# Optimization experiments

Measured on AMD Instinct MI355X. Metric: run time of the kernel, lower is better.

Reference implementation:

```python
import jax, jax.numpy as jnp
import numpy as np

C = 256

def setup_inputs() -> dict:
    key = jax.random.key(0)
    ks = jax.random.split(key, 7)
    s = 1.0 / np.sqrt(C)
    x = jax.random.normal(ks[0], (4, C, 64, 64), dtype=jnp.float32)
    Wq = jax.random.uniform(ks[1], (C, C), jnp.float32, -s, s)
    bq = jax.random.uniform(ks[2], (C,), jnp.float32, -s, s)
    Wk = jax.random.uniform(ks[3], (C, C), jnp.float32, -s, s)
    bk = jax.random.uniform(ks[4], (C,), jnp.float32, -s, s)
    Wv = jax.random.uniform(ks[5], (C, C), jnp.float32, -s, s)
    bv = jax.random.uniform(ks[6], (C,), jnp.float32, -s, s)
    return {"x": x, "Wq": Wq, "bq": bq, "Wk": Wk, "bk": bk, "Wv": Wv, "bv": bv}

def reference(x, Wq, bq, Wk, bk, Wv, bv):
    B, Cc, H, W = x.shape
    N = H * W
    xf = x.reshape(B, Cc, N)                      # (B, C, N)
    # 1x1 conv == channel linear: out[b,o,n] = sum_c W[o,c] x[b,c,n] + b[o]
    q = jnp.einsum('oc,bcn->bno', Wq, xf) + bq    # (B, N, C)  proj_query^T
    k = jnp.einsum('oc,bcn->bon', Wk, xf) + bk[None, :, None]  # (B, C, N)
    v = jnp.einsum('oc,bcn->bon', Wv, xf) + bv[None, :, None]  # (B, C, N)
    energy = jnp.einsum('bnc,bcm->bnm', q, k)     # (B, N, N)
    attention = jax.nn.softmax(energy, axis=-1)
    # out = V @ attention^T : out[b,c,n] = sum_m v[b,c,m] * attention[b,n,m]
    out = jnp.einsum('bcm,bnm->bcn', v, attention)
    return out.reshape(B, Cc, H, W)
```

## Files before the change

kernel.cpp:

```cpp
#include <hip/hip_runtime.h>
#include <math.h>

#define BB 4
#define CC 256
#define NN 4096
#define KV 64

using half8 = __attribute__((ext_vector_type(8))) _Float16;
using f32x4 = __attribute__((ext_vector_type(4))) float;
using f32x16 = __attribute__((ext_vector_type(16))) float;

__device__ __forceinline__ unsigned short f2h(float f) {
  _Float16 h = (_Float16)f;
  return __builtin_bit_cast(unsigned short, h);
}
__device__ __forceinline__ float h2f(unsigned short u) {
  return (float)__builtin_bit_cast(_Float16, u);
}

#define ASYNC16(g, l)                                                        \
  __builtin_amdgcn_global_load_lds(                                          \
      (const __attribute__((address_space(1))) unsigned int*)(g),            \
      (__attribute__((address_space(3))) unsigned int*)(l), 16, 0, 0)

__device__ __forceinline__ int vt_off(int r, int chunk) {
  return r * 64 + (((chunk ^ r) & 7) << 3);
}

__global__ __launch_bounds__(256) void k_wcast(const float* __restrict__ Wq,
    const float* __restrict__ Wk, const float* __restrict__ Wv,
    unsigned short* __restrict__ Wt) {
  int id = blockIdx.x * 256 + threadIdx.x;
  int pos8 = id & 7, o = (id >> 3) & 255, ks = (id >> 11) & 3, p3 = id >> 13;
  const float* W = p3 == 0 ? Wq : (p3 == 1 ? Wk : Wv);
  int c = ks * 64 + ((pos8 ^ o) & 7) * 8;
  const float* src = W + (size_t)o * CC + c;
  float4 a = *(const float4*)(src);
  float4 b4 = *(const float4*)(src + 4);
  union { unsigned short u[8]; uint4 v4; } pk;
  pk.u[0] = f2h(a.x);  pk.u[1] = f2h(a.y);  pk.u[2] = f2h(a.z);  pk.u[3] = f2h(a.w);
  pk.u[4] = f2h(b4.x); pk.u[5] = f2h(b4.y); pk.u[6] = f2h(b4.z); pk.u[7] = f2h(b4.w);
  *(uint4*)(Wt + (size_t)id * 8) = pk.v4;
}

__global__ __launch_bounds__(512) void k_proj(const float* __restrict__ x,
    const unsigned short* __restrict__ Wt,
    const float* __restrict__ bq, const float* __restrict__ bk,
    const float* __restrict__ bv,
    unsigned short* __restrict__ Q, unsigned short* __restrict__ K,
    unsigned short* __restrict__ V) {
  __shared__ __align__(16) char ps[110848];
  float* xf = (float*)ps;
  unsigned short* xa = (unsigned short*)(ps + 8448);
  unsigned short* wh = (unsigned short*)(ps + 12544);
  int b = blockIdx.y, n0 = blockIdx.x * 32;
  int t = threadIdx.x, w = t >> 6, lane = t & 63, l15 = lane & 15, quad = lane >> 4;

  f32x4 z = {0.f, 0.f, 0.f, 0.f};
  f32x4 acc[3][2][2];
#pragma unroll
  for (int p3 = 0; p3 < 3; ++p3)
#pragma unroll
    for (int ct = 0; ct < 2; ++ct)
#pragma unroll
      for (int mt = 0; mt < 2; ++mt) acc[p3][ct][mt] = z;

  for (int ks = 0; ks < 4; ++ks) {
    if (ks) __syncthreads();
#pragma unroll
    for (int p3 = 0; p3 < 3; ++p3) {
      const char* wb = (const char*)(Wt + (size_t)(p3 * 4 + ks) * 16384);
#pragma unroll
      for (int p = 0; p < 4; ++p) {
        int c = p * 512 + t;
        ASYNC16(wb + c * 16, &wh[p3 * 16384 + (p * 512 + (w << 6)) * 8]);
      }
    }
    {
      int c = t >> 3, nl = (t & 7) * 4;
      float4 v = *(const float4*)(x + ((size_t)b * CC + ks * 64 + c) * NN + n0 + nl);
      float* d = xf + c * 33 + nl;
      d[0] = v.x; d[1] = v.y; d[2] = v.z; d[3] = v.w;
    }
    __syncthreads();
    {
      int n = t >> 4, cb = (t & 15) * 4;
      union { unsigned short u[4]; ushort4 v4; } tmp;
#pragma unroll
      for (int i = 0; i < 4; ++i) tmp.u[i] = f2h(xf[(cb + i) * 33 + n]);
      int ch = cb >> 3;
      *(ushort4*)&xa[n * 64 + (((ch ^ n) & 7) << 3) + (cb & 7)] = tmp.v4;
    }
    __syncthreads();
#pragma unroll
    for (int kc = 0; kc < 2; ++kc) {
      half8 af[2];
#pragma unroll
      for (int mt = 0; mt < 2; ++mt)
        af[mt] = *(const half8*)&xa[vt_off(mt * 16 + l15, kc * 4 + quad)];
#pragma unroll
      for (int p3 = 0; p3 < 3; ++p3)
#pragma unroll
        for (int ct = 0; ct < 2; ++ct) {
          half8 bf = *(const half8*)&wh[p3 * 16384 + vt_off(w * 32 + ct * 16 + l15, kc * 4 + quad)];
#pragma unroll
          for (int mt = 0; mt < 2; ++mt)
            acc[p3][ct][mt] = __builtin_amdgcn_mfma_f32_16x16x32_f16(af[mt], bf, acc[p3][ct][mt], 0, 0, 0);
        }
    }
  }
#pragma unroll
  for (int p3 = 0; p3 < 3; ++p3) {
    const float* bias = p3 == 0 ? bq : (p3 == 1 ? bk : bv);
#pragma unroll
    for (int ct = 0; ct < 2; ++ct) {
      float bv_ = bias[w * 32 + ct * 16 + l15];
#pragma unroll
      for (int mt = 0; mt < 2; ++mt)
#pragma unroll
        for (int r = 0; r < 4; ++r) acc[p3][ct][mt][r] += bv_;
    }
  }
#pragma unroll
  for (int p3 = 0; p3 < 2; ++p3) {
    __syncthreads();
    unsigned short* qo = (unsigned short*)ps;
#pragma unroll
    for (int ct = 0; ct < 2; ++ct)
#pragma unroll
      for (int mt = 0; mt < 2; ++mt)
#pragma unroll
        for (int r = 0; r < 4; ++r)
          qo[(mt * 16 + quad * 4 + r) * 264 + w * 32 + ct * 16 + l15] = f2h(acc[p3][ct][mt][r]);
    __syncthreads();
    unsigned short* outp = (p3 == 0 ? Q : K) + ((size_t)b * NN + n0) * CC;
#pragma unroll
    for (int p = 0; p < 2; ++p) {
      int f = p * 8192 + t * 16;
      int n = f >> 9, off = f & 511;
      *(uint4*)((char*)outp + (size_t)n * 512 + off) =
        *(const uint4*)((const char*)&qo[n * 264] + off);
    }
  }
  {
    __syncthreads();
    unsigned short* vo = (unsigned short*)ps;
#pragma unroll
    for (int ct = 0; ct < 2; ++ct)
#pragma unroll
      for (int mt = 0; mt < 2; ++mt)
#pragma unroll
        for (int r = 0; r < 4; ++r)
          vo[(w * 32 + ct * 16 + l15) * 36 + mt * 16 + quad * 4 + r] = f2h(acc[2][ct][mt][r]);
    __syncthreads();
#pragma unroll
    for (int p = 0; p < 2; ++p) {
      int id = p * 512 + t;
      int o = id >> 2, off = (id & 3) * 16;
      *(uint4*)((char*)(V + ((size_t)b * CC + o) * NN + n0) + off) =
        *(const uint4*)((const char*)&vo[o * 36] + off);
    }
  }
}

__global__ __launch_bounds__(512, 2) void k_flash(const unsigned short* __restrict__ Q,
    const unsigned short* __restrict__ K, const unsigned short* __restrict__ V,
    float* __restrict__ out, unsigned short* __restrict__ opart,
    float* __restrict__ ml, int n_splits) {
  __shared__ __align__(16) char sm[134144];
  unsigned short* kt0 = (unsigned short*)sm;
  unsigned short* kt1 = (unsigned short*)(sm + 32768);
  unsigned short* vt0 = (unsigned short*)(sm + 65536);
  unsigned short* vt1 = (unsigned short*)(sm + 98304);
  float* mx  = (float*)(sm + 131072);
  float* ll_ = (float*)(sm + 133120);

  int b = blockIdx.y, q0 = blockIdx.x * 128, split = blockIdx.z;
  int nt = (NN / KV) / n_splits;
  int t = threadIdx.x, w = t >> 6, lane = t & 63;
  int qn = lane & 31, hi = lane >> 5;
  int qg = w >> 1, kth = w & 1;

  half8 qf[16];
  {
    const unsigned short* qrow = Q + ((size_t)b * NN + q0 + qg * 32 + qn) * CC;
#pragma unroll
    for (int cs = 0; cs < 16; ++cs)
      qf[cs] = *(const half8*)(qrow + cs * 16 + hi * 8);
  }

  f32x16 o_acc[8];
#pragma unroll
  for (int ct = 0; ct < 8; ++ct)
#pragma unroll
    for (int r = 0; r < 16; ++r) o_acc[ct][r] = 0.f;

  f32x16 sa;
  float m_i = -INFINITY, lp = 0.f, pm_carry = -INFINITY;

  int it_beg = split * nt, it_end = it_beg + nt;

  auto dma_k = [&](int it, unsigned short* dst) {
    const char* kb = (const char*)(K + ((size_t)b * NN + it * KV) * CC);
#pragma unroll
    for (int p = 0; p < 4; ++p) {
      int c = p * 512 + t;
      int r = c >> 5, chp = c & 31;
      ASYNC16(kb + r * 512 + ((chp ^ (r & 31)) << 4), &dst[(p * 512 + (w << 6)) * 8]);
    }
  };
  auto dma_v = [&](int it, unsigned short* dst) {
    const char* vb = (const char*)(V + (size_t)b * CC * NN) + it * 128;
#pragma unroll
    for (int p = 0; p < 4; ++p) {
      int c = p * 512 + t;
      int r = c >> 3, chp = c & 7;
      ASYNC16(vb + (size_t)r * 8192 + ((chp ^ (r & 7)) << 4), &dst[(p * 512 + (w << 6)) * 8]);
    }
  };

  auto qkt = [&](const unsigned short* kc) {
#pragma unroll
    for (int r = 0; r < 16; ++r) sa[r] = 0.f;
    __builtin_amdgcn_s_setprio(1);
#pragma unroll
    for (int cs = 0; cs < 16; ++cs) {
      half8 kf = *(const half8*)&kc[(kth * 32 + qn) * 256 + ((((cs * 2 + hi) ^ qn) & 31) << 3)];
      sa = __builtin_amdgcn_mfma_f32_32x32x16_f16(kf, qf[cs], sa, 0, 0, 0);
    }
    __builtin_amdgcn_s_setprio(0);
  };

  auto partial_max = [&](int par) {
    float pm = sa[0];
#pragma unroll
    for (int r = 1; r < 16; ++r) pm = fmaxf(pm, sa[r]);
    pm = fmaxf(pm, __shfl_xor(pm, 32, 64));
    pm_carry = pm;
    if (lane < 32) mx[(par * 2 + kth) * 128 + qg * 32 + lane] = pm;
  };

  unsigned int g0x, g0y, g1x, g1y, g2x, g2y, g3x, g3y;

  auto finish_sm = [&](int prevpar) {
    float prt = mx[(prevpar * 2 + (kth ^ 1)) * 128 + qg * 32 + qn];
    float mtile = fmaxf(pm_carry, prt);
    float mnew = fmaxf(m_i, mtile);
    float alpha = __expf(m_i - mnew);
    m_i = mnew;
    float ls = 0.f;
#pragma unroll
    for (int r = 0; r < 16; ++r) {
      float p = __expf(sa[r] - mnew);
      sa[r] = p;
      ls += p;
    }
    ls += __shfl_xor(ls, 32, 64);
    lp = lp * alpha + ls;
    g0x = (unsigned)f2h(sa[0])  | ((unsigned)f2h(sa[1])  << 16);
    g0y = (unsigned)f2h(sa[2])  | ((unsigned)f2h(sa[3])  << 16);
    g1x = (unsigned)f2h(sa[4])  | ((unsigned)f2h(sa[5])  << 16);
    g1y = (unsigned)f2h(sa[6])  | ((unsigned)f2h(sa[7])  << 16);
    g2x = (unsigned)f2h(sa[8])  | ((unsigned)f2h(sa[9])  << 16);
    g2y = (unsigned)f2h(sa[10]) | ((unsigned)f2h(sa[11]) << 16);
    g3x = (unsigned)f2h(sa[12]) | ((unsigned)f2h(sa[13]) << 16);
    g3y = (unsigned)f2h(sa[14]) | ((unsigned)f2h(sa[15]) << 16);
    if (!__all(alpha == 1.0f)) {
#pragma unroll
      for (int ct = 0; ct < 8; ++ct)
#pragma unroll
        for (int r = 0; r < 16; ++r) o_acc[ct][r] *= alpha;
    }
  };

  auto pv = [&](const unsigned short* vp) {
    __builtin_amdgcn_s_setprio(1);
#pragma unroll
    for (int s = 0; s < 2; ++s) {
      unsigned int ax = s ? g2x : g0x, ay = s ? g2y : g0y;
      unsigned int bx = s ? g3x : g1x, by = s ? g3y : g1y;
      unsigned int vx = hi ? ax : bx, vy = hi ? ay : by;
      unsigned int xx = (unsigned int)__shfl_xor((int)vx, 32, 64);
      unsigned int xy = (unsigned int)__shfl_xor((int)vy, 32, 64);
      union { unsigned int u[4]; half8 h; } bf;
      bf.u[0] = hi ? xx : ax;
      bf.u[1] = hi ? xy : ay;
      bf.u[2] = hi ? bx : xx;
      bf.u[3] = hi ? by : xy;
#pragma unroll
      for (int ct = 0; ct < 8; ++ct) {
        half8 af = *(const half8*)&vp[(ct * 32 + qn) * 64 + ((((kth * 4 + s * 2 + hi) ^ (qn & 7)) & 7) << 3)];
        o_acc[ct] = __builtin_amdgcn_mfma_f32_32x32x16_f16(af, bf.h, o_acc[ct], 0, 0, 0);
      }
    }
    __builtin_amdgcn_s_setprio(0);
  };

  dma_k(it_beg, (it_beg & 1) ? kt1 : kt0);
  dma_v(it_beg, (it_beg & 1) ? vt1 : vt0);
  asm volatile("s_waitcnt vmcnt(4) lgkmcnt(0)" ::: "memory");
  __builtin_amdgcn_s_barrier();
  __builtin_amdgcn_sched_barrier(0);
  {
    int par = it_beg & 1;
    if (it_beg + 1 < it_end) {
      dma_k(it_beg + 1, par ? kt0 : kt1);
      dma_v(it_beg + 1, par ? vt0 : vt1);
    }
    qkt(par ? kt1 : kt0);
    partial_max(par);
  }
  for (int it = it_beg + 1; it < it_end; ++it) {
    int par = it & 1;
    const unsigned short* kcur = par ? kt1 : kt0;
    unsigned short* knxt = par ? kt0 : kt1;
    unsigned short* vprv = par ? vt0 : vt1;
    asm volatile("s_waitcnt vmcnt(4) lgkmcnt(0)" ::: "memory");
    __builtin_amdgcn_s_barrier();
    __builtin_amdgcn_sched_barrier(0);
    if (it + 1 < it_end) dma_k(it + 1, knxt);
    finish_sm(par ^ 1);
    pv(vprv);
    __builtin_amdgcn_sched_barrier(0);
    __builtin_amdgcn_s_barrier();
    __builtin_amdgcn_sched_barrier(0);
    if (it + 1 < it_end) dma_v(it + 1, vprv);
    qkt(kcur);
    partial_max(par);
  }
  __syncthreads();
  {
    int par = (it_end - 1) & 1;
    finish_sm(par);
    pv(par ? vt1 : vt0);
  }

  if (lane < 32) ll_[kth * 128 + qg * 32 + lane] = lp;
  __syncthreads();
  float* od0 = (float*)sm;
  float* od1 = od0 + 32 * 132;
  float* linv = (float*)(sm + 33792);
  if (t < 128) {
    float l = ll_[t] + ll_[128 + t];
    linv[t] = (n_splits == 1) ? 1.0f / l : 1.0f;
  }
  if (n_splits != 1 && kth == 0 && lane < 32) {
    size_t qi = (size_t)q0 + qg * 32 + lane;
    float lt = ll_[qg * 32 + lane] + ll_[128 + qg * 32 + lane];
    ml[((size_t)(split * 2 + 0) * BB + b) * NN + qi] = m_i;
    ml[((size_t)(split * 2 + 1) * BB + b) * NN + qi] = lt;
  }
  __syncthreads();

  float* obf = out + (size_t)b * CC * NN + q0;
  unsigned short* obh = opart + ((size_t)split * BB + b) * CC * NN + q0;
#pragma unroll
  for (int ct = 0; ct < 8; ++ct) {
    float* od = kth ? od1 : od0;
#pragma unroll
    for (int r = 0; r < 16; ++r) {
      int cl = (r & 3) + 8 * (r >> 2) + 4 * hi;
      od[cl * 132 + qg * 32 + qn] = o_acc[ct][r];
    }
    __syncthreads();
    {
      int row = t >> 4, q8 = (t & 15) * 8;
      f32x4 a0 = *(const f32x4*)&od0[row * 132 + q8];
      f32x4 a1 = *(const f32x4*)&od0[row * 132 + q8 + 4];
      f32x4 b0 = *(const f32x4*)&od1[row * 132 + q8];
      f32x4 b1 = *(const f32x4*)&od1[row * 132 + q8 + 4];
      f32x4 l0 = *(const f32x4*)&linv[q8];
      f32x4 l1 = *(const f32x4*)&linv[q8 + 4];
      f32x4 s0, s1;
#pragma unroll
      for (int i = 0; i < 4; ++i) {
        s0[i] = (a0[i] + b0[i]) * l0[i];
        s1[i] = (a1[i] + b1[i]) * l1[i];
      }
      if (n_splits == 1) {
        *(f32x4*)(obf + (size_t)(ct * 32 + row) * NN + q8) = s0;
        *(f32x4*)(obf + (size_t)(ct * 32 + row) * NN + q8 + 4) = s1;
      } else {
        union { unsigned short u[8]; uint4 v4; } tmp;
#pragma unroll
        for (int i = 0; i < 4; ++i) { tmp.u[i] = f2h(s0[i]); tmp.u[4 + i] = f2h(s1[i]); }
        *(uint4*)(obh + (size_t)(ct * 32 + row) * NN + q8) = tmp.v4;
      }
    }
    __syncthreads();
  }
}

__global__ __launch_bounds__(256) void k_merge(const unsigned short* __restrict__ opart,
    const float* __restrict__ ml, float* __restrict__ out) {
  size_t i = ((size_t)blockIdx.x * 256 + threadIdx.x) * 4;
  int n = (int)(i & (NN - 1));
  int b = (int)(i >> 20);
  float4 m1 = *(const float4*)(ml + ((size_t)(0 * BB) + b) * NN + n);
  float4 l1 = *(const float4*)(ml + ((size_t)(1 * BB) + b) * NN + n);
  float4 m2 = *(const float4*)(ml + ((size_t)(2 * BB) + b) * NN + n);
  float4 l2 = *(const float4*)(ml + ((size_t)(3 * BB) + b) * NN + n);
  ushort4 o1 = *(const ushort4*)(opart + i);
  ushort4 o2 = *(const ushort4*)(opart + (size_t)BB * CC * NN + i);
  float4 res;
#define MRG(f, comp) { \
    float M = fmaxf(m1.f, m2.f); \
    float e1 = __expf(m1.f - M), e2 = __expf(m2.f - M); \
    res.f = (e1 * h2f(o1.comp) + e2 * h2f(o2.comp)) / (e1 * l1.f + e2 * l2.f); }
  MRG(x, x) MRG(y, y) MRG(z, z) MRG(w, w)
#undef MRG
  *(float4*)(out + i) = res;
}

extern "C" void kernel_launch(void* const* d_in, const int* in_sizes, int n_in,
                              void* d_out, int out_size, void* d_ws, size_t ws_size,
                              hipStream_t stream) {
  const float* x  = (const float*)d_in[0];
  const float* Wq = (const float*)d_in[1];
  const float* bq = (const float*)d_in[2];
  const float* Wk = (const float*)d_in[3];
  const float* bk = (const float*)d_in[4];
  const float* Wv = (const float*)d_in[5];
  const float* bv = (const float*)d_in[6];
  float* out = (float*)d_out;
  char* ws = (char*)d_ws;
  const size_t MB = 1024 * 1024;
  unsigned short* Qb = (unsigned short*)(ws);
  unsigned short* Kb = (unsigned short*)(ws + 8 * MB);
  unsigned short* Vb = (unsigned short*)(ws + 16 * MB);
  unsigned short* Op = (unsigned short*)(ws + 24 * MB);
  float*          Ml = (float*)(ws + 40 * MB);

  int ns = (ws_size >= 41 * MB) ? 2 : 1;
  unsigned short* Wt = (unsigned short*)(ns == 2 ? ws + 40 * MB + 256 * 1024
                                                 : ws + 24 * MB);

  k_wcast<<<dim3(96), 256, 0, stream>>>(Wq, Wk, Wv, Wt);
  k_proj<<<dim3(128, 4), 512, 0, stream>>>(x, Wt, bq, bk, bv, Qb, Kb, Vb);

  k_flash<<<dim3(32, 4, ns), 512, 0, stream>>>(Qb, Kb, Vb, out, Op, Ml, ns);
  if (ns == 2) k_merge<<<dim3(4096), 256, 0, stream>>>(Op, Ml, out);
}
```

Baseline: 240.4 us.

## Decouple per-wave softmax statistics and adopt lazy rescaling in flash loop

Each of the two key-half waves now keeps its own running max and sum instead of exchanging partial maxima through LDS every tile. The two halves are combined once at the end, and the split-merge kernel is adjusted because partial outputs are now normalized. Rescaling of the accumulator is skipped unless the max grows by more than 8, which trims exp and multiply work. The main loop is rewritten as a simple double-buffered loop with a single barrier per tile. This drops the previous software pipeline that overlapped QK of one tile with softmax and PV of the prior tile, and its fine-grained vmcnt waits, so load latency may be less hidden.

Result: faster. 213.1 us (-11.4%).

```diff
diff --git a/kernel.cpp b/kernel.cpp
--- a/kernel.cpp
+++ b/kernel.cpp
@@ -167,13 +167,13 @@
     const unsigned short* __restrict__ K, const unsigned short* __restrict__ V,
     float* __restrict__ out, unsigned short* __restrict__ opart,
     float* __restrict__ ml, int n_splits) {
-  __shared__ __align__(16) char sm[134144];
+  __shared__ __align__(16) char sm[133120];
   unsigned short* kt0 = (unsigned short*)sm;
   unsigned short* kt1 = (unsigned short*)(sm + 32768);
   unsigned short* vt0 = (unsigned short*)(sm + 65536);
   unsigned short* vt1 = (unsigned short*)(sm + 98304);
-  float* mx  = (float*)(sm + 131072);
-  float* ll_ = (float*)(sm + 133120);
+  float* mm_ = (float*)(sm + 131072);
+  float* ll_ = (float*)(sm + 132096);
 
   int b = blockIdx.y, q0 = blockIdx.x * 128, split = blockIdx.z;
   int nt = (NN / KV) / n_splits;
@@ -195,8 +195,7 @@
 #pragma unroll
     for (int r = 0; r < 16; ++r) o_acc[ct][r] = 0.f;
 
-  f32x16 sa;
-  float m_i = -INFINITY, lp = 0.f, pm_carry = -INFINITY;
+  float m_i = -INFINITY, lp = 0.f;
 
   int it_beg = split * nt, it_end = it_beg + nt;
 
@@ -219,61 +218,64 @@
     }
   };
 
-  auto qkt = [&](const unsigned short* kc) {
+  dma_k(it_beg, (it_beg & 1) ? kt1 : kt0);
+  dma_v(it_beg, (it_beg & 1) ? vt1 : vt0);
+
+  for (int it = it_beg; it < it_end; ++it) {
+    int par = it & 1;
+    const unsigned short* kcur = par ? kt1 : kt0;
+    const unsigned short* vcur = par ? vt1 : vt0;
+
+    __syncthreads();
+
+    if (it + 1 < it_end) {
+      dma_k(it + 1, par ? kt0 : kt1);
+      dma_v(it + 1, par ? vt0 : vt1);
+    }
+
+    f32x16 sa;
 #pragma unroll
     for (int r = 0; r < 16; ++r) sa[r] = 0.f;
     __builtin_amdgcn_s_setprio(1);
 #pragma unroll
     for (int cs = 0; cs < 16; ++cs) {
-      half8 kf = *(const half8*)&kc[(kth * 32 + qn) * 256 + ((((cs * 2 + hi) ^ qn) & 31) << 3)];
+      half8 kf = *(const half8*)&kcur[(kth * 32 + qn) * 256 + ((((cs * 2 + hi) ^ qn) & 31) << 3)];
       sa = __builtin_amdgcn_mfma_f32_32x32x16_f16(kf, qf[cs], sa, 0, 0, 0);
     }
     __builtin_amdgcn_s_setprio(0);
-  };
-
-  auto partial_max = [&](int par) {
+
     float pm = sa[0];
 #pragma unroll
     for (int r = 1; r < 16; ++r) pm = fmaxf(pm, sa[r]);
     pm = fmaxf(pm, __shfl_xor(pm, 32, 64));
-    pm_carry = pm;
-    if (lane < 32) mx[(par * 2 + kth) * 128 + qg * 32 + lane] = pm;
-  };
-
-  unsigned int g0x, g0y, g1x, g1y, g2x, g2y, g3x, g3y;
-
-  auto finish_sm = [&](int prevpar) {
-    float prt = mx[(prevpar * 2 + (kth ^ 1)) * 128 + qg * 32 + qn];
-    float mtile = fmaxf(pm_carry, prt);
-    float mnew = fmaxf(m_i, mtile);
-    float alpha = __expf(m_i - mnew);
-    m_i = mnew;
+    if (!__all(pm <= m_i + 8.0f)) {
+      float mnew = fmaxf(m_i, pm);
+      float alpha = __expf(m_i - mnew);
+      m_i = mnew;
+      lp *= alpha;
+#pragma unroll
+      for (int ct = 0; ct < 8; ++ct)
+#pragma unroll
+        for (int r = 0; r < 16; ++r) o_acc[ct][r] *= alpha;
+    }
     float ls = 0.f;
 #pragma unroll
     for (int r = 0; r < 16; ++r) {
-      float p = __expf(sa[r] - mnew);
+      float p = __expf(sa[r] - m_i);
       sa[r] = p;
       ls += p;
     }
-    ls += __shfl_xor(ls, 32, 64);
-    lp = lp * alpha + ls;
-    g0x = (unsigned)f2h(sa[0])  | ((unsigned)f2h(sa[1])  << 16);
-    g0y = (unsigned)f2h(sa[2])  | ((unsigned)f2h(sa[3])  << 16);
-    g1x = (unsigned)f2h(sa[4])  | ((unsigned)f2h(sa[5])  << 16);
-    g1y = (unsigned)f2h(sa[6])  | ((unsigned)f2h(sa[7])  << 16);
-    g2x = (unsigned)f2h(sa[8])  | ((unsigned)f2h(sa[9])  << 16);
-    g2y = (unsigned)f2h(sa[10]) | ((unsigned)f2h(sa[11]) << 16);
-    g3x = (unsigned)f2h(sa[12]) | ((unsigned)f2h(sa[13]) << 16);
-    g3y = (unsigned)f2h(sa[14]) | ((unsigned)f2h(sa[15]) << 16);
-    if (!__all(alpha == 1.0f)) {
-#pragma unroll
-      for (int ct = 0; ct < 8; ++ct)
-#pragma unroll
-        for (int r = 0; r < 16; ++r) o_acc[ct][r] *= alpha;
-    }
-  };
-
-  auto pv = [&](const unsigned short* vp) {
+    lp += ls;
+
+    unsigned int g0x = (unsigned)f2h(sa[0])  | ((unsigned)f2h(sa[1])  << 16);
+    unsigned int g0y = (unsigned)f2h(sa[2])  | ((unsigned)f2h(sa[3])  << 16);
+    unsigned int g1x = (unsigned)f2h(sa[4])  | ((unsigned)f2h(sa[5])  << 16);
+    unsigned int g1y = (unsigned)f2h(sa[6])  | ((unsigned)f2h(sa[7])  << 16);
+    unsigned int g2x = (unsigned)f2h(sa[8])  | ((unsigned)f2h(sa[9])  << 16);
+    unsigned int g2y = (unsigned)f2h(sa[10]) | ((unsigned)f2h(sa[11]) << 16);
+    unsigned int g3x = (unsigned)f2h(sa[12]) | ((unsigned)f2h(sa[13]) << 16);
+    unsigned int g3y = (unsigned)f2h(sa[14]) | ((unsigned)f2h(sa[15]) << 16);
+
     __builtin_amdgcn_s_setprio(1);
 #pragma unroll
     for (int s = 0; s < 2; ++s) {
@@ -289,66 +291,36 @@
       bf.u[3] = hi ? by : xy;
 #pragma unroll
       for (int ct = 0; ct < 8; ++ct) {
-        half8 af = *(const half8*)&vp[(ct * 32 + qn) * 64 + ((((kth * 4 + s * 2 + hi) ^ (qn & 7)) & 7) << 3)];
+        half8 af = *(const half8*)&vcur[(ct * 32 + qn) * 64 + ((((kth * 4 + s * 2 + hi) ^ (qn & 7)) & 7) << 3)];
         o_acc[ct] = __builtin_amdgcn_mfma_f32_32x32x16_f16(af, bf.h, o_acc[ct], 0, 0, 0);
       }
     }
     __builtin_amdgcn_s_setprio(0);
-  };
-
-  dma_k(it_beg, (it_beg & 1) ? kt1 : kt0);
-  dma_v(it_beg, (it_beg & 1) ? vt1 : vt0);
-  asm volatile("s_waitcnt vmcnt(4) lgkmcnt(0)" ::: "memory");
-  __builtin_amdgcn_s_barrier();
-  __builtin_amdgcn_sched_barrier(0);
-  {
-    int par = it_beg & 1;
-    if (it_beg + 1 < it_end) {
-      dma_k(it_beg + 1, par ? kt0 : kt1);
-      dma_v(it_beg + 1, par ? vt0 : vt1);
-    }
-    qkt(par ? kt1 : kt0);
-    partial_max(par);
-  }
-  for (int it = it_beg + 1; it < it_end; ++it) {
-    int par = it & 1;
-    const unsigned short* kcur = par ? kt1 : kt0;
-    unsigned short* knxt = par ? kt0 : kt1;
-    unsigned short* vprv = par ? vt0 : vt1;
-    asm volatile("s_waitcnt vmcnt(4) lgkmcnt(0)" ::: "memory");
-    __builtin_amdgcn_s_barrier();
-    __builtin_amdgcn_sched_barrier(0);
-    if (it + 1 < it_end) dma_k(it + 1, knxt);
-    finish_sm(par ^ 1);
-    pv(vprv);
-    __builtin_amdgcn_sched_barrier(0);
-    __builtin_amdgcn_s_barrier();
-    __builtin_amdgcn_sched_barrier(0);
-    if (it + 1 < it_end) dma_v(it + 1, vprv);
-    qkt(kcur);
-    partial_max(par);
+  }
+
+  lp += __shfl_xor(lp, 32, 64);
+  if (lane < 32) {
+    mm_[kth * 128 + qg * 32 + lane] = m_i;
+    ll_[kth * 128 + qg * 32 + lane] = lp;
   }
   __syncthreads();
-  {
-    int par = (it_end - 1) & 1;
-    finish_sm(par);
-    pv(par ? vt1 : vt0);
-  }
-
-  if (lane < 32) ll_[kth * 128 + qg * 32 + lane] = lp;
-  __syncthreads();
+  float m_oth = mm_[(kth ^ 1) * 128 + qg * 32 + qn];
+  float l_oth = ll_[(kth ^ 1) * 128 + qg * 32 + qn];
+  float M = fmaxf(m_i, m_oth);
+  float myw = __expf(m_i - M);
+  float lcomb = lp * myw + l_oth * __expf(m_oth - M);
+
   float* od0 = (float*)sm;
   float* od1 = od0 + 32 * 132;
   float* linv = (float*)(sm + 33792);
-  if (t < 128) {
-    float l = ll_[t] + ll_[128 + t];
-    linv[t] = (n_splits == 1) ? 1.0f / l : 1.0f;
-  }
-  if (n_splits != 1 && kth == 0 && lane < 32) {
-    size_t qi = (size_t)q0 + qg * 32 + lane;
-    float lt = ll_[qg * 32 + lane] + ll_[128 + qg * 32 + lane];
-    ml[((size_t)(split * 2 + 0) * BB + b) * NN + qi] = m_i;
-    ml[((size_t)(split * 2 + 1) * BB + b) * NN + qi] = lt;
+  if (kth == 0 && lane < 32) {
+    int q = qg * 32 + lane;
+    linv[q] = 1.0f / lcomb;
+    if (n_splits != 1) {
+      size_t qi = (size_t)q0 + q;
+      ml[((size_t)(split * 2 + 0) * BB + b) * NN + qi] = M;
+      ml[((size_t)(split * 2 + 1) * BB + b) * NN + qi] = lcomb;
+    }
   }
   __syncthreads();
 
@@ -360,7 +332,7 @@
 #pragma unroll
     for (int r = 0; r < 16; ++r) {
       int cl = (r & 3) + 8 * (r >> 2) + 4 * hi;
-      od[cl * 132 + qg * 32 + qn] = o_acc[ct][r];
+      od[cl * 132 + qg * 32 + qn] = o_acc[ct][r] * myw;
     }
     __syncthreads();
     {
@@ -405,8 +377,8 @@
   float4 res;
 #define MRG(f, comp) { \
     float M = fmaxf(m1.f, m2.f); \
-    float e1 = __expf(m1.f - M), e2 = __expf(m2.f - M); \
-    res.f = (e1 * h2f(o1.comp) + e2 * h2f(o2.comp)) / (e1 * l1.f + e2 * l2.f); }
+    float e1 = __expf(m1.f - M) * l1.f, e2 = __expf(m2.f - M) * l2.f; \
+    res.f = (e1 * h2f(o1.comp) + e2 * h2f(o2.comp)) / (e1 + e2); }
   MRG(x, x) MRG(y, y) MRG(z, z) MRG(w, w)
 #undef MRG
   *(float4*)(out + i) = res;
```
